# Kernel optimization log

Measured on AMD Instinct MI355X. Metric: run time of the kernel, lower is better.

Reference implementation:

```python
import jax, jax.numpy as jnp
import numpy as np

V, E, D, T, B = 32000, 512, 512, 512, 32
PAD = 3

def layer_norm(x, g, b, eps=1e-5):
    m = jnp.mean(x, axis=-1, keepdims=True)
    v = jnp.mean((x - m) ** 2, axis=-1, keepdims=True)
    return (x - m) * jax.lax.rsqrt(v + eps) * g + b

def sru_direction(U, v, b, reverse):
    # U: (T, B, 4D) -> splits: x_tilde, f-gate pre-act, r-gate pre-act, highway input
    x_t, uf, ur, xp = jnp.split(U, 4, axis=-1)
    def step(c, inp):
        xt, uft, urt, xpt = inp
        f = jax.nn.sigmoid(uft + v[0] * c + b[0])
        r = jax.nn.sigmoid(urt + v[1] * c + b[1])
        c_new = f * c + (1.0 - f) * xt
        h = r * c_new + (1.0 - r) * xpt
        return c_new, h
    c0 = jnp.zeros((U.shape[1], v.shape[1]), U.dtype)  # (B, D)
    c_last, hs = jax.lax.scan(step, c0, (x_t, uf, ur, xp), reverse=reverse)
    return hs, c_last

def setup_inputs() -> dict:
    key = jax.random.key(0)
    ks = jax.random.split(key, 8)
    def rn(k, shp, sc=0.05):
        return jax.random.normal(k, shp, jnp.float32) * sc
    return {
        "src": jax.random.randint(ks[0], (T, B), 0, V),
        "emb": rn(ks[1], (V, E), 0.1),
        "ln_g": jnp.ones((E,), jnp.float32),
        "ln_b": jnp.zeros((E,), jnp.float32),
        "W0": rn(ks[2], (E, 4 * D)),
        "W1": rn(ks[3], (E, 4 * D)),
        "v0": rn(ks[4], (2, D), 0.5),
        "v1": rn(ks[5], (2, D), 0.5),
        "b0": jnp.zeros((2, D), jnp.float32),
        "b1": jnp.zeros((2, D), jnp.float32),
        "W_out": rn(ks[6], (D, 2 * D)),
        "b_out": jnp.zeros((D,), jnp.float32),
    }

def reference(src, emb, ln_g, ln_b, W0, W1, v0, v1, b0, b1, W_out, b_out):
    table = emb.at[PAD].set(0.0)          # padding_idx row is zero
    x = table[src]                         # (T, B, E); dropout p=0 -> identity
    xn = layer_norm(x, ln_g, ln_b)         # SRU layer_norm=True: LN on cell input
    h0, c0 = sru_direction(jnp.einsum('tbe,ef->tbf', xn, W0), v0, b0, False)
    h1, c1 = sru_direction(jnp.einsum('tbe,ef->tbf', xn, W1), v1, b1, True)
    outputs = jnp.concatenate([h0, h1], axis=-1)        # (T, B, 2D)
    hidden = jnp.concatenate([c0, c1], axis=-1)[None]   # (1, B, 2D)
    out = jnp.tanh(jnp.einsum('tbh,dh->tbd', outputs, W_out) + b_out)
    return out, hidden
```

## Files before the change

kernel.cpp:

```cpp
#include <hip/hip_runtime.h>
#include <cstdint>
#include <cstddef>

#define T_DIM 512
#define B_DIM 32
#define E_DIM 512
#define D_DIM 512
#define PAD_IDX 3
#define M_ROWS (T_DIM * B_DIM)
#define PF 32

typedef __attribute__((ext_vector_type(8))) __bf16 bf16x8;
typedef __attribute__((ext_vector_type(4))) float  f32x4;

__device__ __forceinline__ unsigned short f2bf(float x) {
    union { float f; uint32_t u; } v; v.f = x;
    uint32_t u = v.u;
    uint32_t r = (u + 0x7FFFu + ((u >> 16) & 1u)) >> 16;
    return (unsigned short)r;
}
__device__ __forceinline__ float bf2f(unsigned short h) {
    union { float f; uint32_t u; } v; v.u = ((uint32_t)h) << 16;
    return v.f;
}
__device__ __forceinline__ float fast_sigmoid(float z) {
    return __builtin_amdgcn_rcpf(1.f + __expf(-z));
}
__device__ __forceinline__ float fast_tanh(float x) {
    return 1.f - 2.f * __builtin_amdgcn_rcpf(__expf(2.f * x) + 1.f);
}

__global__ __launch_bounds__(256) void prep_kernel(
    const int* __restrict__ src, const float* __restrict__ emb,
    const float* __restrict__ g, const float* __restrict__ bb,
    const float* __restrict__ W0, const float* __restrict__ W1,
    const float* __restrict__ b0, const float* __restrict__ b1,
    const float* __restrict__ W_out,
    unsigned short* __restrict__ xn, unsigned short* __restrict__ Wt,
    unsigned short* __restrict__ Wob, float* __restrict__ bias)
{
    __shared__ float tile[64][65];
    const int bx = blockIdx.x;
    if (bx < 4096) {
        int wave = threadIdx.x >> 6;
        int lane = threadIdx.x & 63;
        int row  = bx * 4 + wave;
        int tok  = src[row];
        float x[8];
        if (tok == PAD_IDX) {
            #pragma unroll
            for (int j = 0; j < 8; j++) x[j] = 0.f;
        } else {
            const float* er = emb + (size_t)tok * E_DIM + lane * 8;
            f32x4 a0 = *(const f32x4*)(er);
            f32x4 a1 = *(const f32x4*)(er + 4);
            #pragma unroll
            for (int j = 0; j < 4; j++) { x[j] = a0[j]; x[4 + j] = a1[j]; }
        }
        float s = 0.f, sq = 0.f;
        #pragma unroll
        for (int j = 0; j < 8; j++) { s += x[j]; sq += x[j] * x[j]; }
        #pragma unroll
        for (int off = 32; off >= 1; off >>= 1) {
            s  += __shfl_xor(s,  off, 64);
            sq += __shfl_xor(sq, off, 64);
        }
        float mean = s * (1.f / 512.f);
        float var  = sq * (1.f / 512.f) - mean * mean;
        float rs   = rsqrtf(var + 1e-5f);
        f32x4 g0 = *(const f32x4*)(g + lane * 8);
        f32x4 g1 = *(const f32x4*)(g + lane * 8 + 4);
        f32x4 c0 = *(const f32x4*)(bb + lane * 8);
        f32x4 c1 = *(const f32x4*)(bb + lane * 8 + 4);
        unsigned short o[8];
        #pragma unroll
        for (int j = 0; j < 4; j++) {
            o[j]     = f2bf((x[j]     - mean) * rs * g0[j] + c0[j]);
            o[4 + j] = f2bf((x[4 + j] - mean) * rs * g1[j] + c1[j]);
        }
        uint4 pk;
        pk.x = (uint32_t)o[0] | ((uint32_t)o[1] << 16);
        pk.y = (uint32_t)o[2] | ((uint32_t)o[3] << 16);
        pk.z = (uint32_t)o[4] | ((uint32_t)o[5] << 16);
        pk.w = (uint32_t)o[6] | ((uint32_t)o[7] << 16);
        *(uint4*)(xn + (size_t)row * E_DIM + lane * 8) = pk;
    } else if (bx < 4608) {
        int bxx = bx - 4096;
        int k0  = (bxx & 7) * 64;
        int n0g = (bxx >> 3) * 64;
        int dir = n0g >> 11;
        const float* W = dir ? W1 : W0;
        int d0 = (n0g & 2047) >> 2;
        int tx = threadIdx.x & 63;
        int ty = threadIdx.x >> 6;
        int scol = ((tx >> 4) << 9) + d0 + (tx & 15);
        for (int r = ty; r < 64; r += 4)
            tile[r][tx] = W[(size_t)(k0 + r) * 2048 + scol];
        __syncthreads();
        for (int r2 = ty; r2 < 64; r2 += 4) {
            int j = ((r2 & 3) << 4) | (r2 >> 2);
            Wt[(size_t)(n0g + r2) * 512 + k0 + tx] = f2bf(tile[tx][j]);
        }
    } else if (bx < 5120) {
        int i = ((bx - 4608) * 256 + threadIdx.x) * 4;
        f32x4 v = *(const f32x4*)(W_out + i);
        uint2 pk;
        pk.x = (uint32_t)f2bf(v[0]) | ((uint32_t)f2bf(v[1]) << 16);
        pk.y = (uint32_t)f2bf(v[2]) | ((uint32_t)f2bf(v[3]) << 16);
        *(uint2*)(Wob + i) = pk;
    } else {
        int n = (bx - 5120) * 256 + threadIdx.x;
        int dir = n >> 11, gg = n & 3, d = (n & 2047) >> 2;
        const float* bp = dir ? b1 : b0;
        float v = (gg == 1) ? bp[d] : ((gg == 2) ? bp[512 + d] : 0.f);
        bias[n] = v;
    }
}

template<int KD, int NMT, int NNT, int GM, int GN, int EPI>
__global__ __launch_bounds__(512, 4) void gemm_pipe_kernel(
    const unsigned short* __restrict__ A,
    const unsigned short* __restrict__ Bt,
    void* __restrict__ Cout,
    const float* __restrict__ bias,
    int ldc)
{
    constexpr int BM = 128, BN = 256;
    constexpr int MR = 4, NR = 4;
    constexpr int NKT = KD / 32;
    constexpr int RA  = BM / 128;
    constexpr int RB  = BN / 128;
    constexpr int LPT = RA + RB;
    constexpr int ASZ = BM * 32;
    constexpr int BSZ = BN * 32;
    __shared__ unsigned short smem[3 * (ASZ + BSZ)];

    const int tid = threadIdx.x;
    const int w   = tid >> 6;
    const int l   = tid & 63;

    constexpr int PER_G = GM * GN;
    constexpr int NGC   = NNT / GN;
    const int bid = blockIdx.x;
    const int c   = bid & 7;
    const int idx = bid >> 3;
    const int gi  = idx / PER_G;
    const int wi  = idx % PER_G;
    const int gg  = c + 8 * gi;
    const int mt  = (gg / NGC) * GM + wi / GN;
    const int nt  = (gg % NGC) * GN + wi % GN;

    const int wm = w >> 2, wn = w & 3;

    const unsigned short* Ab = A  + (size_t)mt * BM * KD;
    const unsigned short* Bb = Bt + (size_t)nt * BN * KD;

    const int srow = w * 16 + (l >> 2);
    const int scol = ((l & 3) ^ ((l >> 3) & 3)) * 8;

    auto stage = [&](int t, int slot) {
        const unsigned short* Ag = Ab + t * 32;
        const unsigned short* Bg = Bb + t * 32;
        unsigned short* As = smem + slot * (ASZ + BSZ);
        unsigned short* Bs = As + ASZ;
        #pragma unroll
        for (int r = 0; r < RA; r++)
            __builtin_amdgcn_global_load_lds(
                (const __attribute__((address_space(1))) void*)(Ag + (size_t)(r * 128 + srow) * KD + scol),
                (__attribute__((address_space(3))) void*)(As + (r * 128 + w * 16) * 32),
                16, 0, 0);
        #pragma unroll
        for (int r = 0; r < RB; r++)
            __builtin_amdgcn_global_load_lds(
                (const __attribute__((address_space(1))) void*)(Bg + (size_t)(r * 128 + srow) * KD + scol),
                (__attribute__((address_space(3))) void*)(Bs + (r * 128 + w * 16) * 32),
                16, 0, 0);
    };

    f32x4 acc[MR][NR];
    #pragma unroll
    for (int m = 0; m < MR; m++)
        #pragma unroll
        for (int n = 0; n < NR; n++)
            acc[m][n] = (f32x4){0.f, 0.f, 0.f, 0.f};

    stage(0, 0); stage(1, 1);

    const int li   = l & 15;
    const int cg   = l >> 4;
    const int rswz = (cg ^ ((li >> 1) & 3)) * 8;

    #pragma unroll
    for (int t = 0; t < NKT; t++) {
        if (t + 1 < NKT)
            asm volatile("s_waitcnt vmcnt(%0) lgkmcnt(0)" :: "n"(LPT) : "memory");
        else
            asm volatile("s_waitcnt vmcnt(0) lgkmcnt(0)" ::: "memory");
        __builtin_amdgcn_s_barrier();
        if (t + 2 < NKT) stage(t + 2, (t + 2) % 3);

        const unsigned short* As = smem + (t % 3) * (ASZ + BSZ);
        const unsigned short* Bs = As + ASZ;
        bf16x8 af[MR], bfv[NR];
        #pragma unroll
        for (int m = 0; m < MR; m++) {
            int row = wm * 64 + m * 16 + li;
            af[m] = *(const bf16x8*)(As + row * 32 + rswz);
        }
        #pragma unroll
        for (int n = 0; n < NR; n++) {
            int row = wn * 64 + n * 16 + li;
            bfv[n] = *(const bf16x8*)(Bs + row * 32 + rswz);
        }
        __builtin_amdgcn_s_setprio(1);
        #pragma unroll
        for (int m = 0; m < MR; m++)
            #pragma unroll
            for (int n = 0; n < NR; n++)
                acc[m][n] = __builtin_amdgcn_mfma_f32_16x16x32_bf16(
                    af[m], bfv[n], acc[m][n], 0, 0, 0);
        __builtin_amdgcn_s_setprio(0);
    }

    const int colb = nt * BN + wn * 64;
    const int rowb = mt * BM + wm * 64;
    #pragma unroll
    for (int m = 0; m < MR; m++) {
        #pragma unroll
        for (int n = 0; n < NR; n++) {
            int col  = colb + n * 16 + li;
            int row0 = rowb + m * 16 + cg * 4;
            float bi = bias[col];
            if (EPI == 0) {
                unsigned short* C = (unsigned short*)Cout;
                #pragma unroll
                for (int j = 0; j < 4; j++)
                    C[(size_t)(row0 + j) * ldc + col] = f2bf(acc[m][n][j] + bi);
            } else {
                float* C = (float*)Cout;
                #pragma unroll
                for (int j = 0; j < 4; j++)
                    C[(size_t)(row0 + j) * ldc + col] = fast_tanh(acc[m][n][j] + bi);
            }
        }
    }
}

__global__ __launch_bounds__(64) void sru_scan_kernel(
    const unsigned short* __restrict__ U,
    const float* __restrict__ v0, const float* __restrict__ v1,
    unsigned short* __restrict__ h,
    float* __restrict__ hidden)
{
    int id  = blockIdx.x * 64 + threadIdx.x;
    int dir = id >> 14;
    int rem = id & 16383;
    int b   = rem >> 9;
    int d   = rem & 511;
    const float* v = dir ? v1 : v0;
    float vf = v[d], vr = v[D_DIM + d];

    int row0  = (dir ? (T_DIM - 1) * B_DIM : 0) + b;
    long step = (long)(dir ? -B_DIM : B_DIM) * 1024;

    const ushort4* lp = (const ushort4*)U + (size_t)row0 * 1024 + dir * 512 + d;
    unsigned short* hp = h + (size_t)row0 * 1024 + dir * 512 + d;

    ushort4 buf[PF];
    #pragma unroll
    for (int p = 0; p < PF; p++) { buf[p] = *lp; lp += step; }

    float c = 0.f;
    for (int tb = 0; tb < T_DIM - PF; tb += PF) {
        #pragma unroll
        for (int p = 0; p < PF; p++) {
            ushort4 q = buf[p];
            buf[p] = *lp; lp += step;
            float x  = bf2f(q.x);
            float uf = bf2f(q.y);
            float ur = bf2f(q.z);
            float xp = bf2f(q.w);
            float f = fast_sigmoid(__fmaf_rn(vf, c, uf));
            float r = fast_sigmoid(__fmaf_rn(vr, c, ur));
            c = __fmaf_rn(f, c - x, x);
            float hv = __fmaf_rn(r, c - xp, xp);
            *hp = f2bf(hv); hp += step;
        }
    }
    #pragma unroll
    for (int p = 0; p < PF; p++) {
        ushort4 q = buf[p];
        float x  = bf2f(q.x);
        float uf = bf2f(q.y);
        float ur = bf2f(q.z);
        float xp = bf2f(q.w);
        float f = fast_sigmoid(__fmaf_rn(vf, c, uf));
        float r = fast_sigmoid(__fmaf_rn(vr, c, ur));
        c = __fmaf_rn(f, c - x, x);
        float hv = __fmaf_rn(r, c - xp, xp);
        *hp = f2bf(hv); hp += step;
    }
    hidden[b * 1024 + dir * 512 + d] = c;
}

extern "C" void kernel_launch(void* const* d_in, const int* in_sizes, int n_in,
                              void* d_out, int out_size, void* d_ws, size_t ws_size,
                              hipStream_t stream)
{
    const int*   src   = (const int*)  d_in[0];
    const float* emb   = (const float*)d_in[1];
    const float* ln_g  = (const float*)d_in[2];
    const float* ln_b  = (const float*)d_in[3];
    const float* W0    = (const float*)d_in[4];
    const float* W1    = (const float*)d_in[5];
    const float* v0    = (const float*)d_in[6];
    const float* v1    = (const float*)d_in[7];
    const float* b0    = (const float*)d_in[8];
    const float* b1    = (const float*)d_in[9];
    const float* W_out = (const float*)d_in[10];
    const float* b_out = (const float*)d_in[11];

    unsigned short* Wt  = (unsigned short*)d_ws;
    unsigned short* Wob = Wt  + (size_t)4096 * 512;
    unsigned short* xn  = Wob + (size_t)512 * 1024;
    unsigned short* U   = xn  + (size_t)M_ROWS * 512;
    unsigned short* h   = U   + (size_t)M_ROWS * 4096;
    float*          bias4096 = (float*)(h + (size_t)M_ROWS * 1024);

    float* out    = (float*)d_out;
    float* hidden = out + (size_t)M_ROWS * D_DIM;
    (void)out;

    prep_kernel<<<5136, 256, 0, stream>>>(src, emb, ln_g, ln_b, W0, W1,
                                          b0, b1, W_out, xn, Wt, Wob, bias4096);

    gemm_pipe_kernel<512, 128, 16, 8, 4, 0>
        <<<2048, 512, 0, stream>>>(xn, Wt, (void*)U, bias4096, 4096);

    sru_scan_kernel<<<512, 64, 0, stream>>>(U, v0, v1, h, hidden);

    gemm_pipe_kernel<1024, 128, 2, 8, 2, 1>
        <<<256, 512, 0, stream>>>(h, Wob, (void*)d_out, b_out, 512);
}
```

Baseline: 152.0 us.

## Use 128x128-tile triple-buffered GEMM for output projection

Adds a new GEMM kernel with 128x128 output tiles, 256 threads, a three-slot LDS ring, and direct global-to-LDS loads for the final output projection (h times W_out with tanh). It replaces the earlier pipelined kernel, which used 512-thread blocks and half as many workgroups. The goals are more workgroups across the CUs, higher occupancy (launch bounds of 3 blocks per CU), and a deeper prefetch that hides load latency. The risk is that smaller tiles lower data reuse per block.

Measured after the change: 154.1 us. No clear change (+1.4%).

```diff
diff --git a/kernel.cpp b/kernel.cpp
--- a/kernel.cpp
+++ b/kernel.cpp
@@ -246,6 +246,129 @@
     }
 }
 
+template<int KD, int NMT, int NNT, int GM, int GN, int EPI>
+__global__ __launch_bounds__(256, 3) void gemm_ring3_kernel(
+    const unsigned short* __restrict__ A,
+    const unsigned short* __restrict__ Bt,
+    void* __restrict__ Cout,
+    const float* __restrict__ bias,
+    int ldc)
+{
+    constexpr int NKT = KD / 32;
+    constexpr int LPT = 4;
+    constexpr int SLOT = 8192;
+    __shared__ unsigned short smem[3 * SLOT];
+
+    const int tid = threadIdx.x;
+    const int w   = tid >> 6;
+    const int l   = tid & 63;
+
+    constexpr int PER_G = GM * GN;
+    constexpr int NGC   = NNT / GN;
+    const int bid = blockIdx.x;
+    const int c   = bid & 7;
+    const int idx = bid >> 3;
+    const int gi  = idx / PER_G;
+    const int wi  = idx % PER_G;
+    const int gg  = c + 8 * gi;
+    const int mt  = (gg / NGC) * GM + wi / GN;
+    const int nt  = (gg % NGC) * GN + wi % GN;
+
+    const int wm = w >> 1, wn = w & 1;
+
+    const unsigned short* Ab = A  + (size_t)mt * 128 * KD;
+    const unsigned short* Bb = Bt + (size_t)nt * 128 * KD;
+
+    const int s_colx = (((l & 3) ^ ((l >> 3) & 3)) * 8);
+
+    auto stage = [&](int t, int slot) {
+        const unsigned short* Ag = Ab + t * 32 + s_colx;
+        const unsigned short* Bg = Bb + t * 32 + s_colx;
+        unsigned short* As = smem + slot * SLOT;
+        unsigned short* Bs = As + 4096;
+        #pragma unroll
+        for (int r = 0; r < 2; r++) {
+            int grow = r * 64 + w * 16 + (l >> 2);
+            __builtin_amdgcn_global_load_lds(
+                (const __attribute__((address_space(1))) void*)(Ag + (size_t)grow * KD),
+                (__attribute__((address_space(3))) void*)(As + r * 2048 + w * 512),
+                16, 0, 0);
+            __builtin_amdgcn_global_load_lds(
+                (const __attribute__((address_space(1))) void*)(Bg + (size_t)grow * KD),
+                (__attribute__((address_space(3))) void*)(Bs + r * 2048 + w * 512),
+                16, 0, 0);
+        }
+    };
+
+    f32x4 acc[4][4];
+    #pragma unroll
+    for (int m = 0; m < 4; m++)
+        #pragma unroll
+        for (int n = 0; n < 4; n++)
+            acc[m][n] = (f32x4){0.f, 0.f, 0.f, 0.f};
+
+    stage(0, 0); stage(1, 1);
+
+    const int li   = l & 15;
+    const int cg   = l >> 4;
+    const int rswz = (cg ^ ((li >> 1) & 3)) * 8;
+
+    #pragma unroll
+    for (int t = 0; t < NKT; t++) {
+        if (t + 1 < NKT)
+            asm volatile("s_waitcnt vmcnt(%0) lgkmcnt(0)" :: "n"(LPT) : "memory");
+        else
+            asm volatile("s_waitcnt vmcnt(0) lgkmcnt(0)" ::: "memory");
+        __builtin_amdgcn_s_barrier();
+        if (t + 2 < NKT) stage(t + 2, (t + 2) % 3);
+
+        const unsigned short* As = smem + (t % 3) * SLOT;
+        const unsigned short* Bs = As + 4096;
+        bf16x8 af[4], bfv[4];
+        #pragma unroll
+        for (int m = 0; m < 4; m++) {
+            int row = wm * 64 + m * 16 + li;
+            af[m] = *(const bf16x8*)(As + row * 32 + rswz);
+        }
+        #pragma unroll
+        for (int n = 0; n < 4; n++) {
+            int row = wn * 64 + n * 16 + li;
+            bfv[n] = *(const bf16x8*)(Bs + row * 32 + rswz);
+        }
+        __builtin_amdgcn_s_setprio(1);
+        #pragma unroll
+        for (int m = 0; m < 4; m++)
+            #pragma unroll
+            for (int n = 0; n < 4; n++)
+                acc[m][n] = __builtin_amdgcn_mfma_f32_16x16x32_bf16(
+                    af[m], bfv[n], acc[m][n], 0, 0, 0);
+        __builtin_amdgcn_s_setprio(0);
+    }
+
+    const int colb = nt * 128 + wn * 64;
+    const int rowb = mt * 128 + wm * 64;
+    #pragma unroll
+    for (int m = 0; m < 4; m++) {
+        #pragma unroll
+        for (int n = 0; n < 4; n++) {
+            int col  = colb + n * 16 + li;
+            int row0 = rowb + m * 16 + cg * 4;
+            float bi = bias[col];
+            if (EPI == 0) {
+                unsigned short* C = (unsigned short*)Cout;
+                #pragma unroll
+                for (int j = 0; j < 4; j++)
+                    C[(size_t)(row0 + j) * ldc + col] = f2bf(acc[m][n][j] + bi);
+            } else {
+                float* C = (float*)Cout;
+                #pragma unroll
+                for (int j = 0; j < 4; j++)
+                    C[(size_t)(row0 + j) * ldc + col] = fast_tanh(acc[m][n][j] + bi);
+            }
+        }
+    }
+}
+
 __global__ __launch_bounds__(64) void sru_scan_kernel(
     const unsigned short* __restrict__ U,
     const float* __restrict__ v0, const float* __restrict__ v1,
@@ -339,6 +462,6 @@
 
     sru_scan_kernel<<<512, 64, 0, stream>>>(U, v0, v1, h, hidden);
 
-    gemm_pipe_kernel<1024, 128, 2, 8, 2, 1>
-        <<<256, 512, 0, stream>>>(h, Wob, (void*)d_out, b_out, 512);
-}
+    gemm_ring3_kernel<1024, 128, 4, 8, 2, 1>
+        <<<512, 256, 0, stream>>>(h, Wob, (void*)d_out, b_out, 512);
+}
```

## Process two M-tiles per GEMM block with mid-pipeline epilogue and vectorized stores

Applied to the files above, without the earlier changes.

The first GEMM now assigns two consecutive 128-row M tiles to each block (half as many blocks), streaming both through one continuous k-pipeline. The first tile's epilogue is written mid-loop while loads for the second tile are already in flight. Swapping the MFMA operands transposes the accumulator layout, so each lane writes 4 contiguous columns as one vector store instead of scattered scalar stores. The trade-off is fewer blocks for occupancy and hand-tuned vmcnt wait counts that must match the in-flight loads exactly.

New measurement: 226.3 us. 48.9% more time.

```diff
diff --git a/kernel.cpp b/kernel.cpp
--- a/kernel.cpp
+++ b/kernel.cpp
@@ -117,7 +117,7 @@
     }
 }
 
-template<int KD, int NMT, int NNT, int GM, int GN, int EPI>
+template<int KD, int TPB, int NMU, int NNT, int GM, int GN, int EPI>
 __global__ __launch_bounds__(512, 4) void gemm_pipe_kernel(
     const unsigned short* __restrict__ A,
     const unsigned short* __restrict__ Bt,
@@ -127,10 +127,8 @@
 {
     constexpr int BM = 128, BN = 256;
     constexpr int MR = 4, NR = 4;
-    constexpr int NKT = KD / 32;
-    constexpr int RA  = BM / 128;
-    constexpr int RB  = BN / 128;
-    constexpr int LPT = RA + RB;
+    constexpr int NKT1 = KD / 32;
+    constexpr int NKT  = NKT1 * TPB;
     constexpr int ASZ = BM * 32;
     constexpr int BSZ = BN * 32;
     __shared__ unsigned short smem[3 * (ASZ + BSZ)];
@@ -147,30 +145,31 @@
     const int gi  = idx / PER_G;
     const int wi  = idx % PER_G;
     const int gg  = c + 8 * gi;
-    const int mt  = (gg / NGC) * GM + wi / GN;
+    const int pt  = (gg / NGC) * GM + wi / GN;
     const int nt  = (gg % NGC) * GN + wi % GN;
+    const int mt0 = pt * TPB;
 
     const int wm = w >> 2, wn = w & 3;
 
-    const unsigned short* Ab = A  + (size_t)mt * BM * KD;
+    const unsigned short* Ab = A  + (size_t)mt0 * BM * KD;
     const unsigned short* Bb = Bt + (size_t)nt * BN * KD;
 
     const int srow = w * 16 + (l >> 2);
     const int scol = ((l & 3) ^ ((l >> 3) & 3)) * 8;
 
     auto stage = [&](int t, int slot) {
-        const unsigned short* Ag = Ab + t * 32;
-        const unsigned short* Bg = Bb + t * 32;
+        const int sub = t / NKT1;
+        const int kt  = t % NKT1;
+        const unsigned short* Ag = Ab + (size_t)sub * BM * KD + kt * 32;
+        const unsigned short* Bg = Bb + kt * 32;
         unsigned short* As = smem + slot * (ASZ + BSZ);
         unsigned short* Bs = As + ASZ;
-        #pragma unroll
-        for (int r = 0; r < RA; r++)
-            __builtin_amdgcn_global_load_lds(
-                (const __attribute__((address_space(1))) void*)(Ag + (size_t)(r * 128 + srow) * KD + scol),
-                (__attribute__((address_space(3))) void*)(As + (r * 128 + w * 16) * 32),
-                16, 0, 0);
-        #pragma unroll
-        for (int r = 0; r < RB; r++)
+        __builtin_amdgcn_global_load_lds(
+            (const __attribute__((address_space(1))) void*)(Ag + (size_t)srow * KD + scol),
+            (__attribute__((address_space(3))) void*)(As + (w * 16) * 32),
+            16, 0, 0);
+        #pragma unroll
+        for (int r = 0; r < 2; r++)
             __builtin_amdgcn_global_load_lds(
                 (const __attribute__((address_space(1))) void*)(Bg + (size_t)(r * 128 + srow) * KD + scol),
                 (__attribute__((address_space(3))) void*)(Bs + (r * 128 + w * 16) * 32),
@@ -190,10 +189,43 @@
     const int cg   = l >> 4;
     const int rswz = (cg ^ ((li >> 1) & 3)) * 8;
 
+    const int colb = nt * BN + wn * 64;
+
+    auto epi = [&](int sub) {
+        const int rowb = (mt0 + sub) * BM + wm * 64;
+        #pragma unroll
+        for (int n = 0; n < NR; n++) {
+            const int col0 = colb + n * 16 + cg * 4;
+            f32x4 bv = *(const f32x4*)(bias + col0);
+            #pragma unroll
+            for (int m = 0; m < MR; m++) {
+                const int row = rowb + m * 16 + li;
+                if (EPI == 0) {
+                    unsigned short* C = (unsigned short*)Cout;
+                    uint2 pk;
+                    pk.x = (uint32_t)f2bf(acc[m][n][0] + bv[0]) |
+                           ((uint32_t)f2bf(acc[m][n][1] + bv[1]) << 16);
+                    pk.y = (uint32_t)f2bf(acc[m][n][2] + bv[2]) |
+                           ((uint32_t)f2bf(acc[m][n][3] + bv[3]) << 16);
+                    *(uint2*)(C + (size_t)row * ldc + col0) = pk;
+                } else {
+                    float* C = (float*)Cout;
+                    f32x4 o;
+                    #pragma unroll
+                    for (int j = 0; j < 4; j++)
+                        o[j] = fast_tanh(acc[m][n][j] + bv[j]);
+                    *(f32x4*)(C + (size_t)row * ldc + col0) = o;
+                }
+            }
+        }
+    };
+
     #pragma unroll
     for (int t = 0; t < NKT; t++) {
-        if (t + 1 < NKT)
-            asm volatile("s_waitcnt vmcnt(%0) lgkmcnt(0)" :: "n"(LPT) : "memory");
+        if (TPB == 2 && (t == NKT1 || t == NKT1 + 1))
+            asm volatile("s_waitcnt vmcnt(19) lgkmcnt(0)" ::: "memory");
+        else if (t + 1 < NKT)
+            asm volatile("s_waitcnt vmcnt(3) lgkmcnt(0)" ::: "memory");
         else
             asm volatile("s_waitcnt vmcnt(0) lgkmcnt(0)" ::: "memory");
         __builtin_amdgcn_s_barrier();
@@ -218,32 +250,20 @@
             #pragma unroll
             for (int n = 0; n < NR; n++)
                 acc[m][n] = __builtin_amdgcn_mfma_f32_16x16x32_bf16(
-                    af[m], bfv[n], acc[m][n], 0, 0, 0);
+                    bfv[n], af[m], acc[m][n], 0, 0, 0);
         __builtin_amdgcn_s_setprio(0);
+
+        if (TPB == 2 && t == NKT1 - 1) {
+            epi(0);
+            #pragma unroll
+            for (int m = 0; m < MR; m++)
+                #pragma unroll
+                for (int n = 0; n < NR; n++)
+                    acc[m][n] = (f32x4){0.f, 0.f, 0.f, 0.f};
+        }
     }
 
-    const int colb = nt * BN + wn * 64;
-    const int rowb = mt * BM + wm * 64;
-    #pragma unroll
-    for (int m = 0; m < MR; m++) {
-        #pragma unroll
-        for (int n = 0; n < NR; n++) {
-            int col  = colb + n * 16 + li;
-            int row0 = rowb + m * 16 + cg * 4;
-            float bi = bias[col];
-            if (EPI == 0) {
-                unsigned short* C = (unsigned short*)Cout;
-                #pragma unroll
-                for (int j = 0; j < 4; j++)
-                    C[(size_t)(row0 + j) * ldc + col] = f2bf(acc[m][n][j] + bi);
-            } else {
-                float* C = (float*)Cout;
-                #pragma unroll
-                for (int j = 0; j < 4; j++)
-                    C[(size_t)(row0 + j) * ldc + col] = fast_tanh(acc[m][n][j] + bi);
-            }
-        }
-    }
+    epi(TPB - 1);
 }
 
 __global__ __launch_bounds__(64) void sru_scan_kernel(
@@ -334,11 +354,11 @@
     prep_kernel<<<5136, 256, 0, stream>>>(src, emb, ln_g, ln_b, W0, W1,
                                           b0, b1, W_out, xn, Wt, Wob, bias4096);
 
-    gemm_pipe_kernel<512, 128, 16, 8, 4, 0>
-        <<<2048, 512, 0, stream>>>(xn, Wt, (void*)U, bias4096, 4096);
+    gemm_pipe_kernel<512, 2, 64, 16, 4, 4, 0>
+        <<<1024, 512, 0, stream>>>(xn, Wt, (void*)U, bias4096, 4096);
 
     sru_scan_kernel<<<512, 64, 0, stream>>>(U, v0, v1, h, hidden);
 
-    gemm_pipe_kernel<1024, 128, 2, 8, 2, 1>
+    gemm_pipe_kernel<1024, 1, 128, 2, 8, 2, 1>
         <<<256, 512, 0, stream>>>(h, Wob, (void*)d_out, b_out, 512);
 }
```
